# Performance work log

Measured on AMD Instinct MI355X. Metric: run time of the kernel, lower is better.

The kernel has to match this reference:

```python
import jax, jax.numpy as jnp
import numpy as np

B, S = 2, 2048
HQ, HKV, D = 32, 8, 128
SCALING = 0.08838834764831845  # 1/sqrt(128)
E4M3_MAX = 448.0
FP4_MAX = 6.0
# e2m1 representable magnitudes and decision midpoints
FP4_GRID = jnp.array([0.0, 0.5, 1.0, 1.5, 2.0, 3.0, 4.0, 6.0], dtype=jnp.float32)
FP4_MID = (FP4_GRID[:-1] + FP4_GRID[1:]) / 2.0


def quant_dequant_e4m3(x):
    """Simulate torch .to(float8_e4m3fn): clamp to +-448, round mantissa to 3 bits."""
    ax = jnp.abs(x)
    xc = jnp.clip(x, -E4M3_MAX, E4M3_MAX)
    e = jnp.clip(jnp.floor(jnp.log2(jnp.maximum(ax, 1e-12))), -6.0, 8.0)
    q = jnp.round(xc * jnp.exp2(3.0 - e)) * jnp.exp2(e - 3.0)
    return jnp.where(ax == 0.0, 0.0, q)


def quant_dequant_fp4(x):
    """FP4 (e2m1) compress/decompress with per-(token,head) absmax scale over head_dim.
    x: [B, S, H, D] -> dequantized [B, S, H, D]."""
    scale = jnp.max(jnp.abs(x), axis=-1, keepdims=True) / FP4_MAX  # [B,S,H,1]
    scale = jnp.maximum(scale, 1e-12)
    xn = x / scale
    idx = jnp.searchsorted(FP4_MID, jnp.abs(xn))  # nearest e2m1 magnitude
    return jnp.sign(xn) * FP4_GRID[idx] * scale


def setup_inputs() -> dict:
    key = jax.random.key(0)
    kq, kk, kv = jax.random.split(key, 3)
    q = jax.random.normal(kq, (B, S, HQ * D), dtype=jnp.float32)
    k = jax.random.normal(kk, (B, S, HKV * D), dtype=jnp.float32)
    v = jax.random.normal(kv, (B, S, HKV * D), dtype=jnp.float32)
    return {"q": q, "k": k, "v": v}


def reference(q, k, v):
    # reshape to heads
    qh = q.reshape(B, S, HQ, D)
    kh = k.reshape(B, S, HKV, D)
    vh = v.reshape(B, S, HKV, D)
    # FP8 cast then FP4 compress/decompress of the KV cache
    kq8 = quant_dequant_e4m3(kh)
    vq8 = quant_dequant_e4m3(vh)
    kd = quant_dequant_fp4(kq8)
    vd = quant_dequant_fp4(vq8)
    # GQA: expand kv heads to query heads
    g = HQ // HKV
    kr = jnp.repeat(kd, g, axis=2)  # [B,S,HQ,D]
    vr = jnp.repeat(vd, g, axis=2)
    scores = jnp.einsum("bqhd,bkhd->bhqk", qh, kr) * SCALING  # [B,HQ,S,S]
    causal = jnp.tril(jnp.ones((S, S), dtype=bool))
    scores = jnp.where(causal[None, None], scores, jnp.float32(-1e30))
    probs = jax.nn.softmax(scores, axis=-1)
    out = jnp.einsum("bhqk,bkhd->bqhd", probs, vr)
    return out.reshape(B, S, HQ * D)
```

## Files before the change

### kernel.cpp

```cpp
#include <hip/hip_runtime.h>
#include <cstdint>
#include <cstddef>

#define B_    2
#define S_    2048
#define HQ_   32
#define HKV_  8
#define D_    128
#define QSCALE_ (0.08838834764831845f * 1.4426950408889634f)

#define NROW_ (B_*S_*HKV_)

typedef __bf16 bf16x8 __attribute__((ext_vector_type(8)));
typedef float  f32x4  __attribute__((ext_vector_type(4)));

__device__ __forceinline__ unsigned short f2bfu(float f) {
    __bf16 b = (__bf16)f;
    return __builtin_bit_cast(unsigned short, b);
}

__device__ __forceinline__ void gl_lds16(const unsigned short* g, unsigned short* l) {
    __builtin_amdgcn_global_load_lds(
        (const __attribute__((address_space(1))) void*)g,
        (__attribute__((address_space(3))) void*)l, 16, 0, 0);
}

__device__ __forceinline__ float qd_e4m3(float x) {
    float ax = fabsf(x);
    float xc = fminf(fmaxf(x, -448.f), 448.f);
    float axc = fmaxf(ax, 1e-12f);
    int e = (int)((__builtin_bit_cast(unsigned int, axc) >> 23) & 255u) - 127;
    e = min(max(e, -6), 8);
    float s1 = __builtin_bit_cast(float, (unsigned int)(130 - e) << 23);
    float s2 = __builtin_bit_cast(float, (unsigned int)(124 + e) << 23);
    float q = rintf(xc * s1) * s2;
    return ax == 0.f ? 0.f : q;
}

__device__ __forceinline__ float qd_fp4(float x, float scale) {
    float xn = x / scale;
    float a = fabsf(xn);
    float g;
    if      (a <= 0.25f) g = 0.f;
    else if (a <= 0.75f) g = 0.5f;
    else if (a <= 1.25f) g = 1.f;
    else if (a <= 1.75f) g = 1.5f;
    else if (a <= 2.5f)  g = 2.f;
    else if (a <= 3.5f)  g = 3.f;
    else if (a <= 5.f)   g = 4.f;
    else                 g = 6.f;
    return copysignf(g * scale, xn);
}

__global__ __launch_bounds__(256) void quant_kv(const float* __restrict__ k,
                                                const float* __restrict__ v,
                                                unsigned short* __restrict__ kd,
                                                unsigned short* __restrict__ vd) {
    int gw = (blockIdx.x * 256 + threadIdx.x) >> 6;
    int lane = threadIdx.x & 63;
    int row = gw;
    const float* src;
    unsigned short* dst;
    if (row < NROW_) { src = k; dst = kd; }
    else             { row -= NROW_; src = v; dst = vd; }
    int b   = row / (S_ * HKV_);
    int rem = row - b * (S_ * HKV_);
    int s   = rem >> 3;
    int h   = rem & 7;
    float2 x = *(const float2*)(src + (size_t)row * D_ + 2 * lane);
    float q0 = qd_e4m3(x.x);
    float q1 = qd_e4m3(x.y);
    float amax = fmaxf(fabsf(q0), fabsf(q1));
#pragma unroll
    for (int m = 1; m < 64; m <<= 1) amax = fmaxf(amax, __shfl_xor(amax, m, 64));
    float scale = fmaxf(amax / 6.0f, 1e-12f);
    float y0 = qd_fp4(q0, scale);
    float y1 = qd_fp4(q1, scale);
    size_t outOff = ((size_t)(b * HKV_ + h) * S_ + s) * D_ + 2 * lane;
    unsigned int pack = (unsigned int)f2bfu(y0) | ((unsigned int)f2bfu(y1) << 16);
    *(unsigned int*)(dst + outOff) = pack;
}

__global__ __launch_bounds__(256) void transpose_v(const unsigned short* __restrict__ vd,
                                                   unsigned short* __restrict__ vdT) {
    __shared__ alignas(16) unsigned short t[64][136];
    int bh = blockIdx.x >> 5;
    int st = blockIdx.x & 31;
    int s0 = st * 64;
    int tid = threadIdx.x;
    {
        int row = tid >> 2;
        const unsigned short* sp = vd + ((size_t)bh * S_ + s0 + row) * D_;
#pragma unroll
        for (int i = 0; i < 4; ++i) {
            int c = (tid & 3) + 4 * i;
            *(uint4*)&t[row][c * 8] = *(const uint4*)(sp + c * 8);
        }
    }
    __syncthreads();
    {
        int d = tid >> 1;
        unsigned short* dp = vdT + ((size_t)bh * D_ + d) * S_ + s0;
#pragma unroll
        for (int i = 0; i < 4; ++i) {
            int c = (tid & 1) + 2 * i;
            int so = c * 8;
            unsigned short tmp[8];
#pragma unroll
            for (int e = 0; e < 8; ++e) tmp[e] = t[so + e][d];
            *(uint4*)(dp + so) = *(uint4*)tmp;
        }
    }
}

__global__ __launch_bounds__(256) void attn(const float* __restrict__ q,
                                            const unsigned short* __restrict__ kd,
                                            const unsigned short* __restrict__ vdT,
                                            float* __restrict__ out) {
    int bh = blockIdx.x;
    int yp = blockIdx.y;
    int b  = bh >> 5;
    int hq = bh & 31;
    int hkv = hq >> 2;
    int tid  = threadIdx.x;
    int lane = tid & 63;
    int wave = tid >> 6;
    int m16  = lane & 15;
    int g    = lane >> 4;
    int m8   = m16 & 7;

    __shared__ alignas(16) unsigned short ks[64 * 128];
    __shared__ alignas(16) unsigned short vs[128 * 64];
    __shared__ alignas(16) unsigned short ps[8 * 16 * 64];

    const unsigned short* kbase = kd  + (size_t)(b * HKV_ + hkv) * S_ * D_;
    const unsigned short* vbase = vdT + (size_t)(b * HKV_ + hkv) * D_ * S_;

    bf16x8 vones;
#pragma unroll
    for (int j = 0; j < 8; ++j) vones[j] = (__bf16)1.0f;

    for (int phase = 0; phase < 2; ++phase) {
        int qt = phase ? yp : (15 - yp);
        int q0 = qt * 128;
        int qs0 = q0 + wave * 32;
        int ktot = 2 * qt + 2;

        bf16x8 qf[2][4];
#pragma unroll
        for (int s = 0; s < 2; ++s) {
            const float* qp = q + (((size_t)b * S_ + (qs0 + s * 16 + m16)) * HQ_ + hq) * D_;
#pragma unroll
            for (int c = 0; c < 4; ++c) {
                const float* p0 = qp + c * 32 + g * 8;
                bf16x8 f;
#pragma unroll
                for (int j = 0; j < 8; ++j) f[j] = (__bf16)(p0[j] * QSCALE_);
                qf[s][c] = f;
            }
        }

        f32x4 o[2][8];
#pragma unroll
        for (int s = 0; s < 2; ++s)
#pragma unroll
            for (int i = 0; i < 8; ++i) o[s][i] = (f32x4){0.f, 0.f, 0.f, 0.f};
        f32x4 o9[2];
        o9[0] = (f32x4){0.f, 0.f, 0.f, 0.f};
        o9[1] = (f32x4){0.f, 0.f, 0.f, 0.f};

        for (int kt = 0; kt < ktot; ++kt) {
            int k0 = kt * 64;
            __syncthreads();
#pragma unroll
            for (int i = 0; i < 4; ++i) {
                int row = wave * 16 + i * 4 + (lane >> 4);
                int c = (lane & 15) ^ (row & 15);
                gl_lds16(kbase + (size_t)(k0 + row) * D_ + c * 8,
                         &ks[wave * 2048 + i * 512]);
            }
#pragma unroll
            for (int i = 0; i < 4; ++i) {
                int d = wave * 32 + i * 8 + (lane >> 3);
                int c = (lane & 7) ^ (d & 7);
                gl_lds16(vbase + (size_t)d * S_ + k0 + c * 8,
                         &vs[wave * 2048 + i * 512]);
            }
            __syncthreads();

            int dq0 = qs0 - k0;
            int e0 = dq0 + 15;
            int e1 = dq0 + 31;
            int nmax0 = min(4, max(0, (e0 >> 4) + 1));
            int nmax1 = min(4, max(0, (e1 >> 4) + 1));
            int kc0   = min(2, max(0, (e0 >> 5) + 1));
            int kc1   = min(2, max(0, (e1 >> 5) + 1));

            f32x4 sa[2][4];
#pragma unroll
            for (int s = 0; s < 2; ++s)
#pragma unroll
                for (int n = 0; n < 4; ++n) sa[s][n] = (f32x4){0.f, 0.f, 0.f, 0.f};
#pragma unroll
            for (int n = 0; n < 4; ++n) {
                if (n < nmax1) {
#pragma unroll
                    for (int c = 0; c < 4; ++c) {
                        bf16x8 ak = *(const bf16x8*)&ks[(n * 16 + m16) * 128 +
                                                        (((c * 4 + g) ^ m16) * 8)];
                        if (n < nmax0)
                            sa[0][n] = __builtin_amdgcn_mfma_f32_16x16x32_bf16(ak, qf[0][c], sa[0][n], 0, 0, 0);
                        sa[1][n] = __builtin_amdgcn_mfma_f32_16x16x32_bf16(ak, qf[1][c], sa[1][n], 0, 0, 0);
                    }
                }
            }

#pragma unroll
            for (int s = 0; s < 2; ++s) {
                int nmx = s ? nmax1 : nmax0;
                int kcm = s ? kc1 : kc0;
                int dqs = dq0 + s * 16;
#pragma unroll
                for (int n = 0; n < 4; ++n) {
                    if (n < 2 * kcm) {
                        uint2 val; val.x = 0u; val.y = 0u;
                        if (n < nmx) {
                            bool needMask = (n * 16 + 15 > dqs);
                            float pr[4];
#pragma unroll
                            for (int r = 0; r < 4; ++r) {
                                float p = exp2f(sa[s][n][r]);
                                if (needMask)
                                    p = (n * 16 + g * 4 + r <= dqs + m16) ? p : 0.f;
                                pr[r] = p;
                            }
                            val.x = (unsigned int)f2bfu(pr[0]) | ((unsigned int)f2bfu(pr[1]) << 16);
                            val.y = (unsigned int)f2bfu(pr[2]) | ((unsigned int)f2bfu(pr[3]) << 16);
                        }
                        int chunk = (n * 2 + (g >> 1)) ^ m8;
                        *(uint2*)&ps[(wave * 2 + s) * 1024 + m16 * 64 + chunk * 8 + (g & 1) * 4] = val;
                    }
                }
            }
            asm volatile("s_waitcnt lgkmcnt(0)" ::: "memory");

            bf16x8 pa[2][2];
#pragma unroll
            for (int s = 0; s < 2; ++s) {
                int kcm = s ? kc1 : kc0;
#pragma unroll
                for (int kc = 0; kc < 2; ++kc)
                    if (kc < kcm)
                        pa[s][kc] = *(const bf16x8*)&ps[(wave * 2 + s) * 1024 + m16 * 64 +
                                                        (((kc * 4 + g) ^ m8) * 8)];
            }
#pragma unroll
            for (int kc = 0; kc < 2; ++kc) {
                if (kc < kc0)
                    o9[0] = __builtin_amdgcn_mfma_f32_16x16x32_bf16(pa[0][kc], vones, o9[0], 0, 0, 0);
                if (kc < kc1)
                    o9[1] = __builtin_amdgcn_mfma_f32_16x16x32_bf16(pa[1][kc], vones, o9[1], 0, 0, 0);
            }
#pragma unroll
            for (int ds = 0; ds < 8; ++ds) {
#pragma unroll
                for (int kc = 0; kc < 2; ++kc) {
                    if (kc < kc1) {
                        bf16x8 vb = *(const bf16x8*)&vs[(ds * 16 + m16) * 64 +
                                                        (((kc * 4 + g) ^ m8) * 8)];
                        if (kc < kc0)
                            o[0][ds] = __builtin_amdgcn_mfma_f32_16x16x32_bf16(pa[0][kc], vb, o[0][ds], 0, 0, 0);
                        o[1][ds] = __builtin_amdgcn_mfma_f32_16x16x32_bf16(pa[1][kc], vb, o[1][ds], 0, 0, 0);
                    }
                }
            }
        }

#pragma unroll
        for (int s = 0; s < 2; ++s)
#pragma unroll
            for (int r = 0; r < 4; ++r) {
                float inv = 1.f / o9[s][r];
                float* op = out + (((size_t)b * S_ + (qs0 + s * 16 + g * 4 + r)) * HQ_ + hq) * D_;
#pragma unroll
                for (int ds = 0; ds < 8; ++ds)
                    op[ds * 16 + m16] = o[s][ds][r] * inv;
            }
    }
}

extern "C" void kernel_launch(void* const* d_in, const int* in_sizes, int n_in,
                              void* d_out, int out_size, void* d_ws, size_t ws_size,
                              hipStream_t stream) {
    const float* q = (const float*)d_in[0];
    const float* k = (const float*)d_in[1];
    const float* v = (const float*)d_in[2];
    float* out = (float*)d_out;

    unsigned short* kd  = (unsigned short*)d_ws;
    unsigned short* vd  = kd + (size_t)NROW_ * D_;
    unsigned short* vdT = vd + (size_t)NROW_ * D_;

    quant_kv<<<16384, 256, 0, stream>>>(k, v, kd, vd);
    transpose_v<<<512, 256, 0, stream>>>(vd, vdT);
    attn<<<dim3(64, 8), 256, 0, stream>>>(q, kd, vdT, out);
}
```

Before: 266.2 us.

## Double-buffer K/V tiles in LDS to overlap global loads with MFMA compute

```diff
diff --git a/kernel.cpp b/kernel.cpp
--- a/kernel.cpp
+++ b/kernel.cpp
@@ -129,8 +129,8 @@
     int g    = lane >> 4;
     int m8   = m16 & 7;
 
-    __shared__ alignas(16) unsigned short ks[64 * 128];
-    __shared__ alignas(16) unsigned short vs[128 * 64];
+    __shared__ alignas(16) unsigned short ks[2 * 64 * 128];
+    __shared__ alignas(16) unsigned short vs[2 * 128 * 64];
     __shared__ alignas(16) unsigned short ps[8 * 16 * 64];
 
     const unsigned short* kbase = kd  + (size_t)(b * HKV_ + hkv) * S_ * D_;
@@ -169,25 +169,39 @@
         o9[0] = (f32x4){0.f, 0.f, 0.f, 0.f};
         o9[1] = (f32x4){0.f, 0.f, 0.f, 0.f};
 
+        const unsigned short* kp[4];
+        const unsigned short* vp[4];
+#pragma unroll
+        for (int i = 0; i < 4; ++i) {
+            int row = wave * 16 + i * 4 + (lane >> 4);
+            kp[i] = kbase + (size_t)row * D_ + (((lane & 15) ^ (row & 15)) * 8);
+            int d = wave * 32 + i * 8 + (lane >> 3);
+            vp[i] = vbase + (size_t)d * S_ + (((lane & 7) ^ (d & 7)) * 8);
+        }
+
+#pragma unroll
+        for (int i = 0; i < 4; ++i) gl_lds16(kp[i], &ks[wave * 2048 + i * 512]);
+#pragma unroll
+        for (int i = 0; i < 4; ++i) gl_lds16(vp[i], &vs[wave * 2048 + i * 512]);
+#pragma unroll
+        for (int i = 0; i < 4; ++i) { kp[i] += 64 * D_; vp[i] += 64; }
+
         for (int kt = 0; kt < ktot; ++kt) {
+            int cur = kt & 1;
+            int curK = cur * 8192, curV = cur * 8192;
+            __syncthreads();
+
+            if (kt + 1 < ktot) {
+                int nxt = (1 - cur) * 8192;
+#pragma unroll
+                for (int i = 0; i < 4; ++i) gl_lds16(kp[i], &ks[nxt + wave * 2048 + i * 512]);
+#pragma unroll
+                for (int i = 0; i < 4; ++i) gl_lds16(vp[i], &vs[nxt + wave * 2048 + i * 512]);
+#pragma unroll
+                for (int i = 0; i < 4; ++i) { kp[i] += 64 * D_; vp[i] += 64; }
+            }
+
             int k0 = kt * 64;
-            __syncthreads();
-#pragma unroll
-            for (int i = 0; i < 4; ++i) {
-                int row = wave * 16 + i * 4 + (lane >> 4);
-                int c = (lane & 15) ^ (row & 15);
-                gl_lds16(kbase + (size_t)(k0 + row) * D_ + c * 8,
-                         &ks[wave * 2048 + i * 512]);
-            }
-#pragma unroll
-            for (int i = 0; i < 4; ++i) {
-                int d = wave * 32 + i * 8 + (lane >> 3);
-                int c = (lane & 7) ^ (d & 7);
-                gl_lds16(vbase + (size_t)d * S_ + k0 + c * 8,
-                         &vs[wave * 2048 + i * 512]);
-            }
-            __syncthreads();
-
             int dq0 = qs0 - k0;
             int e0 = dq0 + 15;
             int e1 = dq0 + 31;
@@ -206,7 +220,7 @@
                 if (n < nmax1) {
 #pragma unroll
                     for (int c = 0; c < 4; ++c) {
-                        bf16x8 ak = *(const bf16x8*)&ks[(n * 16 + m16) * 128 +
+                        bf16x8 ak = *(const bf16x8*)&ks[curK + (n * 16 + m16) * 128 +
                                                         (((c * 4 + g) ^ m16) * 8)];
                         if (n < nmax0)
                             sa[0][n] = __builtin_amdgcn_mfma_f32_16x16x32_bf16(ak, qf[0][c], sa[0][n], 0, 0, 0);
@@ -266,7 +280,7 @@
 #pragma unroll
                 for (int kc = 0; kc < 2; ++kc) {
                     if (kc < kc1) {
-                        bf16x8 vb = *(const bf16x8*)&vs[(ds * 16 + m16) * 64 +
+                        bf16x8 vb = *(const bf16x8*)&vs[curV + (ds * 16 + m16) * 64 +
                                                         (((kc * 4 + g) ^ m8) * 8)];
                         if (kc < kc0)
                             o[0][ds] = __builtin_amdgcn_mfma_f32_16x16x32_bf16(pa[0][kc], vb, o[0][ds], 0, 0, 0);
```

Result: slower. 386.0 us (+45.0%).
